# Performance work log

Measured on AMD Instinct MI355X. Metric: run time of the kernel, lower is better.

The kernel has to match this reference:

```python
import jax, jax.numpy as jnp
import numpy as np

N_EMBD = 512
HEAD_SIZE = 64
T = 4096
B = 4


def setup_inputs() -> dict:
    key = jax.random.key(0)
    kx, kq, kk, kv = jax.random.split(key, 4)
    x = jax.random.normal(kx, (B, T, N_EMBD), dtype=jnp.float32)
    # torch nn.Linear(n_embd, head_size, bias=False): weight [head_size, n_embd];
    # stored here transposed as [n_embd, head_size] so projection is x @ W.
    s = 1.0 / np.sqrt(N_EMBD)
    Wq = jax.random.uniform(kq, (N_EMBD, HEAD_SIZE), jnp.float32, -s, s)
    Wk = jax.random.uniform(kk, (N_EMBD, HEAD_SIZE), jnp.float32, -s, s)
    Wv = jax.random.uniform(kv, (N_EMBD, HEAD_SIZE), jnp.float32, -s, s)
    return {"x": x, "Wq": Wq, "Wk": Wk, "Wv": Wv}


def reference(x, Wq, Wk, Wv):
    Bq, Tq, C = x.shape
    q = x @ Wq  # [B,T,H]
    k = x @ Wk  # [B,T,H]
    v = x @ Wv  # [B,T,H]
    # NOTE: original scales by C**-0.5 with C = n_embd (input dim), not head_size.
    wei = jnp.einsum('bqh,bkh->bqk', q, k) * (C ** -0.5)  # [B,T,T]
    causal = jnp.tril(jnp.ones((Tq, Tq), dtype=bool))
    wei = jnp.where(causal, wei, -jnp.inf)
    wei = jax.nn.softmax(wei, axis=-1)
    # dropout p=0.0 -> identity (eval-mode deterministic baseline)
    out = jnp.einsum('bqk,bkh->bqh', wei, v)  # [B,T,H]
    return out
```

## Files before the change

### kernel.cpp

```cpp
#include <hip/hip_runtime.h>
#include <hip/hip_bf16.h>
#include <math.h>

#define T_SEQ 4096
#define NBATCH 4
#define C_EMB 512
#define HEAD 64
#define CHUNK 8
#define EPB 288

typedef __attribute__((ext_vector_type(8))) short short8;
typedef __attribute__((ext_vector_type(4))) float f32x4;

#define C2 (0.044194173824159216f * 1.44269504088896340736f)

__device__ __forceinline__ unsigned short f2bf(float f) {
    union { float f; unsigned u; } v; v.f = f;
    unsigned u = v.u;
    u += 0x7FFF + ((u >> 16) & 1);
    return (unsigned short)(u >> 16);
}
__device__ __forceinline__ unsigned pk2bf(float a, float b) {
    __hip_bfloat162 h = __float22bfloat162_rn(make_float2(a, b));
    return *(unsigned*)&h;
}

__global__ __launch_bounds__(64) void wcvt_kernel(
    const float* __restrict__ Wq, const float* __restrict__ Wk,
    const float* __restrict__ Wv, unsigned short* __restrict__ wt)
{
    const int w = blockIdx.x >> 6;
    const int n = blockIdx.x & 63;
    const float* W = (w == 0) ? Wq : (w == 1) ? Wk : Wv;
    const int k0 = threadIdx.x * 8;
    unsigned short tmp[8];
#pragma unroll
    for (int i = 0; i < 8; ++i) tmp[i] = f2bf(W[(size_t)(k0 + i) * HEAD + n]);
    *(short8*)(wt + ((size_t)blockIdx.x) * C_EMB + k0) = *(short8*)tmp;
}

__device__ __forceinline__ void ld_stage(const float* xp, int s, float4* xr) {
#pragma unroll
    for (int j = 0; j < 4; ++j) {
        xr[2 * j]     = *(const float4*)(xp + (s * 4 + j) * 32);
        xr[2 * j + 1] = *(const float4*)(xp + (s * 4 + j) * 32 + 4);
    }
}

__device__ __forceinline__ void mm_stage(const float4* xr, int s, int l16, int quad,
                                         const unsigned short* __restrict__ wt,
                                         f32x4 acc[3][4]) {
#pragma unroll
    for (int j = 0; j < 4; ++j) {
        const int kc = s * 4 + j;
        float4 a = xr[2 * j], b = xr[2 * j + 1];
        int4 ai = make_int4((int)pk2bf(a.x, a.y), (int)pk2bf(a.z, a.w),
                            (int)pk2bf(b.x, b.y), (int)pk2bf(b.z, b.w));
        short8 af = *(short8*)&ai;
#pragma unroll
        for (int w = 0; w < 3; ++w)
#pragma unroll
            for (int n = 0; n < 4; ++n) {
                short8 bf = *(const short8*)(wt + ((size_t)(w * 64 + n * 16 + l16)) * C_EMB
                                                + kc * 32 + quad * 8);
                acc[w][n] = __builtin_amdgcn_mfma_f32_16x16x32_bf16(af, bf, acc[w][n], 0, 0, 0);
            }
    }
}

__global__ __launch_bounds__(256) void proj_kernel(
    const float* __restrict__ x,
    const unsigned short* __restrict__ wt,
    unsigned short* __restrict__ qout,
    unsigned short* __restrict__ kout,
    unsigned short* __restrict__ vt)
{
    __shared__ unsigned short Vsh[64][72];

    const int tid  = threadIdx.x;
    const int wave = tid >> 6;
    const int lane = tid & 63;
    const int l16  = lane & 15;
    const int quad = lane >> 4;
    const int row0 = blockIdx.x * 64;
    const int rowW = row0 + wave * 16 + l16;

    f32x4 acc[3][4];
#pragma unroll
    for (int w = 0; w < 3; ++w)
#pragma unroll
        for (int n = 0; n < 4; ++n) acc[w][n] = (f32x4){0.f, 0.f, 0.f, 0.f};

    const float* xp = x + (size_t)rowW * C_EMB + quad * 8;
    float4 xr[2][8];
    ld_stage(xp, 0, xr[0]);
#pragma unroll
    for (int s = 0; s < 4; ++s) {
        if (s < 3) ld_stage(xp, s + 1, xr[(s + 1) & 1]);
        mm_stage(xr[s & 1], s, l16, quad, wt, acc);
    }

#pragma unroll
    for (int n = 0; n < 4; ++n)
#pragma unroll
        for (int r = 0; r < 4; ++r) {
            int row = row0 + wave * 16 + quad * 4 + r;
            qout[(size_t)row * HEAD + n * 16 + l16] = f2bf(acc[0][n][r] * C2);
            kout[(size_t)row * HEAD + n * 16 + l16] = f2bf(acc[1][n][r]);
        }

#pragma unroll
    for (int n = 0; n < 4; ++n)
#pragma unroll
        for (int r = 0; r < 4; ++r)
            Vsh[n * 16 + l16][wave * 16 + quad * 4 + r] = f2bf(acc[2][n][r]);
    __syncthreads();
    {
        int h  = tid >> 2;
        int tc = (tid & 3) * 16;
        int b  = row0 >> 12;
        int t0 = row0 & (T_SEQ - 1);
        unsigned short* dst = vt + ((size_t)(b * HEAD + h)) * T_SEQ + t0 + tc;
        *(short8*)dst       = *(const short8*)&Vsh[h][tc];
        *(short8*)(dst + 8) = *(const short8*)&Vsh[h][tc + 8];
    }
}

__global__ __launch_bounds__(256) void attn1_kernel(
    const unsigned short* __restrict__ qb,
    const unsigned short* __restrict__ kb,
    const unsigned short* __restrict__ vt,
    float* __restrict__ po,
    float* __restrict__ pl)
{
    __shared__ unsigned short Ks[2][64][72];
    __shared__ unsigned short Vs[2][64][72];
    __shared__ unsigned short Ps[4][16][72];

    const int tid  = threadIdx.x;
    const int wave = tid >> 6;
    const int lane = tid & 63;
    const int l16  = lane & 15;
    const int quad = lane >> 4;

    const int b = blockIdx.x / EPB;
    const int e = blockIdx.x % EPB;
    int g = 0;
#pragma unroll
    for (int gg = 1; gg < 8; ++gg) if (e >= 4 * gg * (gg + 1)) g = gg;
    const int rem = e - 4 * g * (g + 1);
    const int t   = rem / (g + 1);
    const int c   = rem - t * (g + 1);
    const int qt  = 8 * g + t;

    const size_t base = (size_t)b * T_SEQ;
    const int qrow = qt * 64 + wave * 16 + l16;
    short8 aq0 = *(const short8*)(qb + (base + qrow) * HEAD + quad * 8);
    short8 aq1 = *(const short8*)(qb + (base + qrow) * HEAD + 32 + quad * 8);

    float lacc[4];
    f32x4 o[4];
#pragma unroll
    for (int r = 0; r < 4; ++r) lacc[r] = 0.f;
#pragma unroll
    for (int n = 0; n < 4; ++n) o[n] = (f32x4){0.f, 0.f, 0.f, 0.f};

    const int kt0 = c * CHUNK;
    const int kt1 = min(kt0 + CHUNK, qt + 1);
    const int np  = kt1 - kt0;

    const int sr = tid >> 2;
    const int sc = (tid & 3) * 16;

    short8 kra, krb, vra, vrb;
    {
        const int kbase = kt0 * 64;
        const unsigned short* ksrc = kb + (base + kbase + sr) * HEAD + sc;
        const unsigned short* vsrc = vt + ((size_t)(b * HEAD + sr)) * T_SEQ + kbase + sc;
        kra = *(const short8*)(ksrc);     krb = *(const short8*)(ksrc + 8);
        vra = *(const short8*)(vsrc);     vrb = *(const short8*)(vsrc + 8);
    }
    *(short8*)&Ks[0][sr][sc]     = kra;  *(short8*)&Ks[0][sr][sc + 8] = krb;
    *(short8*)&Vs[0][sr][sc]     = vra;  *(short8*)&Vs[0][sr][sc + 8] = vrb;

    for (int p = 0; p < np; ++p) {
        const int cur = p & 1;
        const int kbase = (kt0 + p) * 64;
        __syncthreads();

        if (p + 1 < np) {
            const int nb = kbase + 64;
            const unsigned short* ksrc = kb + (base + nb + sr) * HEAD + sc;
            const unsigned short* vsrc = vt + ((size_t)(b * HEAD + sr)) * T_SEQ + nb + sc;
            kra = *(const short8*)(ksrc);  krb = *(const short8*)(ksrc + 8);
            vra = *(const short8*)(vsrc);  vrb = *(const short8*)(vsrc + 8);
        }

        f32x4 s[4];
#pragma unroll
        for (int n = 0; n < 4; ++n) {
            f32x4 accS = (f32x4){0.f, 0.f, 0.f, 0.f};
            short8 bk0 = *(const short8*)&Ks[cur][n * 16 + l16][quad * 8];
            short8 bk1 = *(const short8*)&Ks[cur][n * 16 + l16][32 + quad * 8];
            accS = __builtin_amdgcn_mfma_f32_16x16x32_bf16(aq0, bk0, accS, 0, 0, 0);
            accS = __builtin_amdgcn_mfma_f32_16x16x32_bf16(aq1, bk1, accS, 0, 0, 0);
            s[n] = accS;
        }

#pragma unroll
        for (int n = 0; n < 4; ++n)
#pragma unroll
            for (int r = 0; r < 4; ++r)
                s[n][r] = __builtin_amdgcn_exp2f(s[n][r]);

        if (kbase + 64 > qt * 64) {
#pragma unroll
            for (int r = 0; r < 4; ++r) {
                int grow = qt * 64 + wave * 16 + quad * 4 + r;
#pragma unroll
                for (int n = 0; n < 4; ++n)
                    if (kbase + n * 16 + l16 > grow) s[n][r] = 0.f;
            }
        }

#pragma unroll
        for (int r = 0; r < 4; ++r)
            lacc[r] += (s[0][r] + s[1][r]) + (s[2][r] + s[3][r]);

#pragma unroll
        for (int n = 0; n < 4; n += 2)
#pragma unroll
            for (int r = 0; r < 4; ++r) {
                unsigned u = pk2bf(s[n][r], s[n + 1][r]);
                Ps[wave][quad * 4 + r][n * 16 + l16]       = (unsigned short)u;
                Ps[wave][quad * 4 + r][(n + 1) * 16 + l16] = (unsigned short)(u >> 16);
            }

        short8 ap0 = *(const short8*)&Ps[wave][l16][quad * 8];
        short8 ap1 = *(const short8*)&Ps[wave][l16][32 + quad * 8];
#pragma unroll
        for (int n = 0; n < 4; ++n) {
            short8 bv0 = *(const short8*)&Vs[cur][n * 16 + l16][quad * 8];
            short8 bv1 = *(const short8*)&Vs[cur][n * 16 + l16][32 + quad * 8];
            o[n] = __builtin_amdgcn_mfma_f32_16x16x32_bf16(ap0, bv0, o[n], 0, 0, 0);
            o[n] = __builtin_amdgcn_mfma_f32_16x16x32_bf16(ap1, bv1, o[n], 0, 0, 0);
        }

        if (p + 1 < np) {
            const int nxt = cur ^ 1;
            *(short8*)&Ks[nxt][sr][sc]     = kra;  *(short8*)&Ks[nxt][sr][sc + 8] = krb;
            *(short8*)&Vs[nxt][sr][sc]     = vra;  *(short8*)&Vs[nxt][sr][sc + 8] = vrb;
        }
    }

#pragma unroll
    for (int off = 1; off < 16; off <<= 1)
#pragma unroll
        for (int r = 0; r < 4; ++r)
            lacc[r] += __shfl_xor(lacc[r], off);

    const int pid = blockIdx.x;
#pragma unroll
    for (int n = 0; n < 4; ++n)
#pragma unroll
        for (int r = 0; r < 4; ++r) {
            int lr = wave * 16 + quad * 4 + r;
            po[(size_t)pid * 4096 + lr * 64 + n * 16 + l16] = o[n][r];
        }
    if (l16 == 0) {
#pragma unroll
        for (int r = 0; r < 4; ++r) {
            int lr = wave * 16 + quad * 4 + r;
            pl[pid * 64 + lr] = lacc[r];
        }
    }
}

__global__ __launch_bounds__(256) void combine_kernel(
    const float* __restrict__ po, const float* __restrict__ pl,
    float* __restrict__ out)
{
    const int gth = blockIdx.x * 256 + threadIdx.x;
    const int h4  = gth & 15;
    const int row = gth >> 4;
    const int lr  = row & 63;
    const int qt  = (row >> 6) & 63;
    const int b   = row >> 12;
    const int nc  = (qt >> 3) + 1;
    const int g   = qt >> 3;
    const int rem = qt & 7;
    const int e0  = 4 * g * (g + 1) + rem * (g + 1);
    const int pid0 = b * EPB + e0;

    float l = 0.f;
    float4 acc = make_float4(0.f, 0.f, 0.f, 0.f);
    for (int cc = 0; cc < nc; ++cc) {
        l += pl[(pid0 + cc) * 64 + lr];
        float4 p4 = *(const float4*)(po + (size_t)(pid0 + cc) * 4096 + lr * 64 + h4 * 4);
        acc.x += p4.x; acc.y += p4.y; acc.z += p4.z; acc.w += p4.w;
    }
    float inv = 1.f / l;
    float4 res = make_float4(acc.x * inv, acc.y * inv, acc.z * inv, acc.w * inv);
    *(float4*)(out + (size_t)gth * 4) = res;
}

extern "C" void kernel_launch(void* const* d_in, const int* in_sizes, int n_in,
                              void* d_out, int out_size, void* d_ws, size_t ws_size,
                              hipStream_t stream) {
    const float* x  = (const float*)d_in[0];
    const float* Wq = (const float*)d_in[1];
    const float* Wk = (const float*)d_in[2];
    const float* Wv = (const float*)d_in[3];
    float* out = (float*)d_out;

    char* ws = (char*)d_ws;
    unsigned short* qb = (unsigned short*)(ws);
    unsigned short* kb = (unsigned short*)(ws + (2u << 20));
    unsigned short* vt = (unsigned short*)(ws + (4u << 20));
    unsigned short* wt = (unsigned short*)(ws + (6u << 20));
    float* pl = (float*)(ws + (6u << 20) + 196608);
    float* po = (float*)(ws + (6u << 20) + 196608 + 294912);

    wcvt_kernel<<<dim3(192), dim3(64), 0, stream>>>(Wq, Wk, Wv, wt);
    proj_kernel<<<dim3(256), dim3(256), 0, stream>>>(x, wt, qb, kb, vt);
    attn1_kernel<<<dim3(NBATCH * EPB), dim3(256), 0, stream>>>(qb, kb, vt, po, pl);
    combine_kernel<<<dim3(1024), dim3(256), 0, stream>>>(po, pl, out);
}
```

Before: 135.3 us.

## Keep softmax probabilities in registers by transposing QK^T MFMA and permuting V staging

The QK^T MFMA operands are swapped so each lane holds scores for one query row across consecutive keys. Those scores can then be packed straight into the A operand of the PV MFMA without going through the shared-memory Ps buffer. V is staged into LDS with a matching column permutation so the key order lines up with the register layout. The row-sum reduction becomes a single scalar per lane with two cross-quad shuffles. This removes the per-iteration LDS write/read round trip for P, at the cost of four narrower LDS stores for V and a less obvious permutation that has to be exactly right for correctness.

Result: faster. 128.4 us (-5.0%).

```diff
diff --git a/kernel.cpp b/kernel.cpp
--- a/kernel.cpp
+++ b/kernel.cpp
@@ -10,6 +10,7 @@
 #define EPB 288
 
 typedef __attribute__((ext_vector_type(8))) short short8;
+typedef __attribute__((ext_vector_type(4))) short short4v;
 typedef __attribute__((ext_vector_type(4))) float f32x4;
 
 #define C2 (0.044194173824159216f * 1.44269504088896340736f)
@@ -126,6 +127,14 @@
     }
 }
 
+__device__ __forceinline__ void stage_v(unsigned short (*Vbuf)[72], int sr, int phiA,
+                                        short8 v0, short8 v1) {
+    *(short4v*)&Vbuf[sr][phiA]      = __builtin_shufflevector(v0, v0, 0, 1, 2, 3);
+    *(short4v*)&Vbuf[sr][phiA + 8]  = __builtin_shufflevector(v0, v0, 4, 5, 6, 7);
+    *(short4v*)&Vbuf[sr][phiA + 16] = __builtin_shufflevector(v1, v1, 0, 1, 2, 3);
+    *(short4v*)&Vbuf[sr][phiA + 24] = __builtin_shufflevector(v1, v1, 4, 5, 6, 7);
+}
+
 __global__ __launch_bounds__(256) void attn1_kernel(
     const unsigned short* __restrict__ qb,
     const unsigned short* __restrict__ kb,
@@ -135,7 +144,6 @@
 {
     __shared__ unsigned short Ks[2][64][72];
     __shared__ unsigned short Vs[2][64][72];
-    __shared__ unsigned short Ps[4][16][72];
 
     const int tid  = threadIdx.x;
     const int wave = tid >> 6;
@@ -158,19 +166,17 @@
     short8 aq0 = *(const short8*)(qb + (base + qrow) * HEAD + quad * 8);
     short8 aq1 = *(const short8*)(qb + (base + qrow) * HEAD + 32 + quad * 8);
 
-    float lacc[4];
+    float lacc = 0.f;
     f32x4 o[4];
 #pragma unroll
-    for (int r = 0; r < 4; ++r) lacc[r] = 0.f;
-#pragma unroll
     for (int n = 0; n < 4; ++n) o[n] = (f32x4){0.f, 0.f, 0.f, 0.f};
 
     const int kt0 = c * CHUNK;
-    const int kt1 = min(kt0 + CHUNK, qt + 1);
-    const int np  = kt1 - kt0;
-
-    const int sr = tid >> 2;
-    const int sc = (tid & 3) * 16;
+    const int np  = min(CHUNK, qt + 1 - kt0);
+
+    const int sr   = tid >> 2;
+    const int sc   = (tid & 3) * 16;
+    const int phiA = (sc & 32) + ((sc & 16) >> 2);
 
     short8 kra, krb, vra, vrb;
     {
@@ -181,7 +187,7 @@
         vra = *(const short8*)(vsrc);     vrb = *(const short8*)(vsrc + 8);
     }
     *(short8*)&Ks[0][sr][sc]     = kra;  *(short8*)&Ks[0][sr][sc + 8] = krb;
-    *(short8*)&Vs[0][sr][sc]     = vra;  *(short8*)&Vs[0][sr][sc + 8] = vrb;
+    stage_v(Vs[0], sr, phiA, vra, vrb);
 
     for (int p = 0; p < np; ++p) {
         const int cur = p & 1;
@@ -199,11 +205,11 @@
         f32x4 s[4];
 #pragma unroll
         for (int n = 0; n < 4; ++n) {
-            f32x4 accS = (f32x4){0.f, 0.f, 0.f, 0.f};
             short8 bk0 = *(const short8*)&Ks[cur][n * 16 + l16][quad * 8];
             short8 bk1 = *(const short8*)&Ks[cur][n * 16 + l16][32 + quad * 8];
-            accS = __builtin_amdgcn_mfma_f32_16x16x32_bf16(aq0, bk0, accS, 0, 0, 0);
-            accS = __builtin_amdgcn_mfma_f32_16x16x32_bf16(aq1, bk1, accS, 0, 0, 0);
+            f32x4 accS = (f32x4){0.f, 0.f, 0.f, 0.f};
+            accS = __builtin_amdgcn_mfma_f32_16x16x32_bf16(bk0, aq0, accS, 0, 0, 0);
+            accS = __builtin_amdgcn_mfma_f32_16x16x32_bf16(bk1, aq1, accS, 0, 0, 0);
             s[n] = accS;
         }
 
@@ -214,50 +220,42 @@
                 s[n][r] = __builtin_amdgcn_exp2f(s[n][r]);
 
         if (kbase + 64 > qt * 64) {
-#pragma unroll
-            for (int r = 0; r < 4; ++r) {
-                int grow = qt * 64 + wave * 16 + quad * 4 + r;
-#pragma unroll
-                for (int n = 0; n < 4; ++n)
-                    if (kbase + n * 16 + l16 > grow) s[n][r] = 0.f;
+            const int cb = kbase + quad * 4;
+#pragma unroll
+            for (int n = 0; n < 4; ++n)
+#pragma unroll
+                for (int r = 0; r < 4; ++r)
+                    if (cb + n * 16 + r > qrow) s[n][r] = 0.f;
+        }
+
+#pragma unroll
+        for (int n = 0; n < 4; ++n)
+            lacc += (s[n][0] + s[n][1]) + (s[n][2] + s[n][3]);
+
+#pragma unroll
+        for (int st = 0; st < 2; ++st) {
+            int4 ai = make_int4(
+                (int)pk2bf(s[2 * st][0],     s[2 * st][1]),
+                (int)pk2bf(s[2 * st][2],     s[2 * st][3]),
+                (int)pk2bf(s[2 * st + 1][0], s[2 * st + 1][1]),
+                (int)pk2bf(s[2 * st + 1][2], s[2 * st + 1][3]));
+            short8 af = *(short8*)&ai;
+#pragma unroll
+            for (int n = 0; n < 4; ++n) {
+                short8 bv = *(const short8*)&Vs[cur][n * 16 + l16][32 * st + quad * 8];
+                o[n] = __builtin_amdgcn_mfma_f32_16x16x32_bf16(af, bv, o[n], 0, 0, 0);
             }
-        }
-
-#pragma unroll
-        for (int r = 0; r < 4; ++r)
-            lacc[r] += (s[0][r] + s[1][r]) + (s[2][r] + s[3][r]);
-
-#pragma unroll
-        for (int n = 0; n < 4; n += 2)
-#pragma unroll
-            for (int r = 0; r < 4; ++r) {
-                unsigned u = pk2bf(s[n][r], s[n + 1][r]);
-                Ps[wave][quad * 4 + r][n * 16 + l16]       = (unsigned short)u;
-                Ps[wave][quad * 4 + r][(n + 1) * 16 + l16] = (unsigned short)(u >> 16);
-            }
-
-        short8 ap0 = *(const short8*)&Ps[wave][l16][quad * 8];
-        short8 ap1 = *(const short8*)&Ps[wave][l16][32 + quad * 8];
-#pragma unroll
-        for (int n = 0; n < 4; ++n) {
-            short8 bv0 = *(const short8*)&Vs[cur][n * 16 + l16][quad * 8];
-            short8 bv1 = *(const short8*)&Vs[cur][n * 16 + l16][32 + quad * 8];
-            o[n] = __builtin_amdgcn_mfma_f32_16x16x32_bf16(ap0, bv0, o[n], 0, 0, 0);
-            o[n] = __builtin_amdgcn_mfma_f32_16x16x32_bf16(ap1, bv1, o[n], 0, 0, 0);
         }
 
         if (p + 1 < np) {
             const int nxt = cur ^ 1;
             *(short8*)&Ks[nxt][sr][sc]     = kra;  *(short8*)&Ks[nxt][sr][sc + 8] = krb;
-            *(short8*)&Vs[nxt][sr][sc]     = vra;  *(short8*)&Vs[nxt][sr][sc + 8] = vrb;
-        }
-    }
-
-#pragma unroll
-    for (int off = 1; off < 16; off <<= 1)
-#pragma unroll
-        for (int r = 0; r < 4; ++r)
-            lacc[r] += __shfl_xor(lacc[r], off);
+            stage_v(Vs[nxt], sr, phiA, vra, vrb);
+        }
+    }
+
+    lacc += __shfl_xor(lacc, 16);
+    lacc += __shfl_xor(lacc, 32);
 
     const int pid = blockIdx.x;
 #pragma unroll
@@ -267,13 +265,8 @@
             int lr = wave * 16 + quad * 4 + r;
             po[(size_t)pid * 4096 + lr * 64 + n * 16 + l16] = o[n][r];
         }
-    if (l16 == 0) {
-#pragma unroll
-        for (int r = 0; r < 4; ++r) {
-            int lr = wave * 16 + quad * 4 + r;
-            pl[pid * 64 + lr] = lacc[r];
-        }
-    }
+    if (quad == 0)
+        pl[pid * 64 + wave * 16 + l16] = lacc;
 }
 
 __global__ __launch_bounds__(256) void combine_kernel(
```
